# Performance work log

Hardware: AMD Instinct MI355X
Metric: run time of the kernel (lower is better)

## Reference

```python
import jax, jax.numpy as jnp
import numpy as np

N = 4096          # n_nodes == batch_size (GFN operates on dense [N,N] adjacency)
E = 65536         # edges per view (avg degree 16)
D = [512, 256, 128]
HV = [128, 64]    # hidden_size_v
HM = [64, 32]     # hidden_size


def _xavier(key, shape):
    fan_in, fan_out = shape[0], shape[1]
    lim = np.sqrt(6.0 / (fan_in + fan_out))
    return jax.random.uniform(key, shape, jnp.float32, -lim, lim)


def setup_inputs() -> dict:
    key = jax.random.key(0)
    ks = jax.random.split(key, 40)
    inp = {}
    inp['data1'] = jax.random.normal(ks[0], (N, D[0]), jnp.float32)
    inp['data2'] = jax.random.normal(ks[1], (N, D[1]), jnp.float32)
    inp['data3'] = jax.random.normal(ks[2], (N, D[2]), jnp.float32)
    # graphs: random edge lists + matching dense adjacency (g.ndata['adj'])
    for v, k_ in zip((1, 2, 3), (ks[3], ks[4], ks[5])):
        ka, kb = jax.random.split(k_)
        src = jax.random.randint(ka, (E,), 0, N, jnp.int32)
        dst = jax.random.randint(kb, (E,), 0, N, jnp.int32)
        adj = np.zeros((N, N), np.float32)
        adj[np.asarray(src), np.asarray(dst)] = 1.0
        inp[f'src{v}'] = src
        inp[f'dst{v}'] = dst
        inp[f'adj{v}'] = jnp.asarray(adj)
    # per-view GraphConv weights (DGL GraphConv: weight [in,out], bias [out])
    dims = {1: [D[0]] + HV, 2: [D[1]] + HV, 3: [D[2]] + HV}
    ki = 6
    for v in (1, 2, 3):
        for l in range(len(HV)):
            inp[f'w{v}_{l}'] = _xavier(ks[ki], (dims[v][l], dims[v][l + 1])); ki += 1
            inp[f'b{v}_{l}'] = jnp.zeros((dims[v][l + 1],), jnp.float32)
    # consensus GraphConv stack
    mdims = [HV[-1]] + HM
    for l in range(len(HM)):
        inp[f'wm_{l}'] = _xavier(ks[ki], (mdims[l], mdims[l + 1])); ki += 1
        inp[f'bm_{l}'] = jnp.zeros((mdims[l + 1],), jnp.float32)
    # FeatureFusion weights [HV[-1], HV[-1]]
    inp['fw1'] = _xavier(ks[ki], (HV[-1], HV[-1])); ki += 1
    inp['fw2'] = _xavier(ks[ki], (HV[-1], HV[-1])); ki += 1
    inp['fw3'] = _xavier(ks[ki], (HV[-1], HV[-1])); ki += 1
    # GFN: Linear(N, N//2) -> ReLU -> Linear(N//2, N); torch Linear weight [out,in]
    H = N // 2
    inp['gfn_w1'] = _xavier(ks[ki], (H, N)); ki += 1
    inp['gfn_b1'] = jnp.zeros((H,), jnp.float32)
    inp['gfn_w2'] = _xavier(ks[ki], (N, H)); ki += 1
    inp['gfn_b2'] = jnp.zeros((N,), jnp.float32)
    return inp


def _gconv(src, dst, x, W, b):
    ones = jnp.ones((src.shape[0],), x.dtype)
    deg_out = jnp.clip(jax.ops.segment_sum(ones, src, num_segments=N), 1.0)
    deg_in = jnp.clip(jax.ops.segment_sum(ones, dst, num_segments=N), 1.0)
    h = (x * jax.lax.rsqrt(deg_out)[:, None]) @ W  # diag norms commute with W
    agg = jax.ops.segment_sum(h[src], dst, num_segments=N)
    return agg * jax.lax.rsqrt(deg_in)[:, None] + b


def _dense_gconv(A, x, W, b):
    # same math on a dense (multigraph-count) adjacency; A[src,dst] counts edges
    deg_out = jnp.clip(A.sum(axis=1), 1.0)
    deg_in = jnp.clip(A.sum(axis=0), 1.0)
    h = (x * jax.lax.rsqrt(deg_out)[:, None]) @ W
    agg = A.T @ h
    return agg * jax.lax.rsqrt(deg_in)[:, None] + b


def reference(data1, data2, data3, src1, dst1, src2, dst2, src3, dst3,
              adj1, adj2, adj3,
              w1_0, b1_0, w1_1, b1_1, w2_0, b2_0, w2_1, b2_1,
              w3_0, b3_0, w3_1, b3_1, wm_0, bm_0, wm_1, bm_1,
              fw1, fw2, fw3, gfn_w1, gfn_b1, gfn_w2, gfn_b2):
    # per-view encoder stacks (relu on all but last layer)
    f1 = jax.nn.relu(_gconv(src1, dst1, data1, w1_0, b1_0))
    f1 = _gconv(src1, dst1, f1, w1_1, b1_1)
    f2 = jax.nn.relu(_gconv(src2, dst2, data2, w2_0, b2_0))
    f2 = _gconv(src2, dst2, f2, w2_1, b2_1)
    f3 = jax.nn.relu(_gconv(src3, dst3, data3, w3_0, b3_0))
    f3 = _gconv(src3, dst3, f3, w3_1, b3_1)
    # FeatureFusion (dropout treated as eval/identity): softmax then relu
    z = f1 @ fw1 + f2 @ fw2 + f3 @ fw3
    z = jax.nn.relu(jax.nn.softmax(z, axis=1))
    # consensus graph: GFN on summed dense adjacency
    adjin = adj1 + adj2 + adj3
    adj_r = jax.nn.relu(adjin @ gfn_w1.T + gfn_b1) @ gfn_w2.T + gfn_b2
    adj_p = jnp.round(jnp.clip(adj_r, 0.0, 1.0) + 0.1)
    # dgl.from_scipy on (adj_p + adj_p.T) keeps edge per nonzero; add_self_loop
    # adds one extra self edge per node -> multigraph edge counts = struct + I
    A = ((adj_p + adj_p.T) != 0).astype(jnp.float32) + jnp.eye(N, dtype=jnp.float32)
    A = jax.lax.stop_gradient(A)  # graph built from detached adj_p
    feat = jax.nn.relu(_dense_gconv(A, z, wm_0, bm_0))
    feat = _dense_gconv(A, feat, wm_1, bm_1)
    # InnerProductDecoder with identity activation (same for every view)
    adj_rec = feat @ feat.T
    return adj_r, adj_rec, feat
```

## Files before the change

kernel.cpp:

```cpp
#include <hip/hip_runtime.h>


#define N_ 4096
#define E_ 65536

typedef __attribute__((ext_vector_type(8))) short short8;
typedef __attribute__((ext_vector_type(4))) float f32x4;

__device__ __forceinline__ float bf2f(unsigned short u) {
  union { unsigned int i; float f; } v; v.i = ((unsigned int)u) << 16; return v.f;
}
__device__ __forceinline__ unsigned short f2bf(float f) {
  union { float f; unsigned int i; } v; v.f = f;
  return (unsigned short)((v.i + 0x7fffu + ((v.i >> 16) & 1u)) >> 16);
}

#define OFF_DEG    0
#define OFF_HX     28672
#define OFF_HBUF   552960
#define OFF_HBUF2  1077248
#define OFF_FV1    1339392
#define OFF_FV2    1601536
#define OFF_FV3    1863680
#define OFF_ZB     2125824
#define OFF_ZPRE   2387968
#define CSR_STRIDE 73732


__global__ void k_count3(const int* __restrict__ s1, const int* __restrict__ d1,
                         const int* __restrict__ s2, const int* __restrict__ d2,
                         const int* __restrict__ s3, const int* __restrict__ d3,
                         float* __restrict__ wd) {
  int v = blockIdx.x >> 8;
  int e = (blockIdx.x & 255) * 256 + threadIdx.x;
  const int* sv = v == 0 ? s1 : (v == 1 ? s2 : s3);
  const int* dv = v == 0 ? d1 : (v == 1 ? d2 : d3);
  atomicAdd(&wd[v * 8192 + sv[e]], 1.f);
  atomicAdd(&wd[v * 8192 + 4096 + dv[e]], 1.f);
}

__global__ void k_rsq(float* __restrict__ p, int n) {
  int i = blockIdx.x * 256 + threadIdx.x;
  if (i < n) p[i] = 1.f / sqrtf(fmaxf(p[i], 1.f));
}

__global__ void k_scan(const float* __restrict__ wd, int* __restrict__ csr) {
  int v = blockIdx.x;
  const float* di = wd + v * 8192 + 4096;
  int* ptr = csr + v * CSR_STRIDE;
  int* cur = ptr + 4100;
  __shared__ int part[256];
  int t = threadIdx.x;
  int local[16];
  int s = 0;
#pragma unroll
  for (int i = 0; i < 16; ++i) { local[i] = s; s += (int)di[t * 16 + i]; }
  part[t] = s;
  __syncthreads();
  for (int o = 1; o < 256; o <<= 1) {
    int x = (t >= o) ? part[t - o] : 0;
    __syncthreads();
    part[t] += x;
    __syncthreads();
  }
  int base = (t > 0) ? part[t - 1] : 0;
#pragma unroll
  for (int i = 0; i < 16; ++i) { ptr[t * 16 + i] = base + local[i]; cur[t * 16 + i] = 0; }
  if (t == 255) ptr[4096] = part[255];
}

__global__ void k_fill(const int* __restrict__ s1, const int* __restrict__ d1,
                       const int* __restrict__ s2, const int* __restrict__ d2,
                       const int* __restrict__ s3, const int* __restrict__ d3,
                       int* __restrict__ csr) {
  int v = blockIdx.x >> 8;
  int e = (blockIdx.x & 255) * 256 + threadIdx.x;
  const int* sv = v == 0 ? s1 : (v == 1 ? s2 : s3);
  const int* dv = v == 0 ? d1 : (v == 1 ? d2 : d3);
  int* ptr = csr + v * CSR_STRIDE;
  int* cur = ptr + 4100;
  int* cidx = cur + 4096;
  int d = dv[e];
  int pos = ptr[d] + atomicAdd(&cur[d], 1);
  cidx[pos] = sv[e];
}

template<int C, int RELU>
__global__ void k_agg(const float* __restrict__ h, const int* __restrict__ csrv,
                      const float* __restrict__ rs, const float* __restrict__ bias,
                      float* __restrict__ out) {
  const int* ptr = csrv;
  const int* cidx = csrv + 4100 + 4096;
  int wave = threadIdx.x >> 6, lane = threadIdx.x & 63;
  int dst, col;
  if (C == 128) { dst = (blockIdx.x << 1) + (wave >> 1); col = ((wave & 1) << 6) + lane; }
  else          { dst = (blockIdx.x << 2) + wave;        col = lane; }
  int e0 = ptr[dst], e1 = ptr[dst + 1];
  float acc = 0.f;
  for (int e = e0; e < e1; ++e) acc += h[(size_t)cidx[e] * C + col];
  float v = acc * rs[dst] + bias[col];
  if (RELU) v = fmaxf(v, 0.f);
  out[(size_t)dst * C + col] = v;
}

__global__ void k_bitset(const int* __restrict__ s1, const int* __restrict__ d1,
                         const int* __restrict__ s2, const int* __restrict__ d2,
                         const int* __restrict__ s3, const int* __restrict__ d3,
                         unsigned* __restrict__ bm) {
  int v = blockIdx.x >> 8;
  int e = (blockIdx.x & 255) * 256 + threadIdx.x;
  const int* sv = v == 0 ? s1 : (v == 1 ? s2 : s3);
  const int* dv = v == 0 ? d1 : (v == 1 ? d2 : d3);
  unsigned idx = (unsigned)sv[e] * 4096u + (unsigned)dv[e];
  atomicOr(&bm[v * 524288 + (idx >> 5)], 1u << (idx & 31));
}

__global__ void k_b2a(const unsigned* __restrict__ bm, ushort* __restrict__ adjin) {
  int i = blockIdx.x * 256 + threadIdx.x;
  int w = i >> 2, sh = (i & 3) << 3;
  unsigned a = bm[w] >> sh, b = bm[524288 + w] >> sh, c = bm[1048576 + w] >> sh;
  short8 o;
#pragma unroll
  for (int k = 0; k < 8; ++k) {
    int cnt = ((a >> k) & 1) + ((b >> k) & 1) + ((c >> k) & 1);
    o[k] = (short)f2bf((float)cnt);
  }
  *(short8*)(adjin + (size_t)i * 8) = o;
}

__global__ void k_split2(const float4* __restrict__ g1, const float4* __restrict__ g2,
                         ushort* __restrict__ w1h, ushort* __restrict__ w1l,
                         ushort* __restrict__ w2h, ushort* __restrict__ w2l) {
  int i = blockIdx.x * 256 + threadIdx.x;
  int hf = i >= 2097152;
  int j = hf ? i - 2097152 : i;
  float4 x = hf ? g2[j] : g1[j];
  ushort* ph = hf ? w2h : w1h;
  ushort* pl = hf ? w2l : w1l;
  ushort4 h, l;
  h.x = f2bf(x.x); l.x = f2bf(x.x - bf2f(h.x));
  h.y = f2bf(x.y); l.y = f2bf(x.y - bf2f(h.y));
  h.z = f2bf(x.z); l.z = f2bf(x.z - bf2f(h.z));
  h.w = f2bf(x.w); l.w = f2bf(x.w - bf2f(h.w));
  *(ushort4*)(ph + (size_t)j * 4) = h;
  *(ushort4*)(pl + (size_t)j * 4) = l;
}

template<int RELU, int WT>
__global__ void k_finalize(const float* __restrict__ agg, const float* __restrict__ rs,
                           const float* __restrict__ bias, float* __restrict__ out,
                           float* __restrict__ outT, int C) {
  int i = blockIdx.x * 256 + threadIdx.x;
  int row = i / C, c = i % C;
  if (row >= N_) return;
  float v = agg[i] * rs[row] + bias[c];
  if (RELU) v = fmaxf(v, 0.f);
  out[i] = v;
  if (WT) outT[(size_t)c * N_ + row] = v;
}

__global__ void k_softmax(const float* __restrict__ zp, float* __restrict__ z) {
  int row = blockIdx.x * 4 + (threadIdx.x >> 6);
  int lane = threadIdx.x & 63;
  float v = zp[row * 64 + lane];
  float m = v;
  for (int o = 32; o; o >>= 1) m = fmaxf(m, __shfl_xor(m, o, 64));
  float e = expf(v - m);
  float s = e;
  for (int o = 32; o; o >>= 1) s += __shfl_xor(s, o, 64);
  z[row * 64 + lane] = e / s;
}

__global__ void k_buildA(const float* __restrict__ adjr, ushort* __restrict__ Ab,
                         float* __restrict__ degA) {
  int bi = blockIdx.y, bj = blockIdx.x;
  __shared__ float t2[64][65];
  int t = threadIdx.x;
  for (int i = 0; i < 16; ++i) {
    int idx = t + i * 256, r = idx >> 6, c = idx & 63;
    t2[r][c] = adjr[(size_t)(bj * 64 + r) * N_ + bi * 64 + c];
  }
  __syncthreads();
  int w = t >> 6, lane = t & 63;
  for (int rr = 0; rr < 16; ++rr) {
    int r = w * 16 + rr;
    int gi = bi * 64 + r, gj = bj * 64 + lane;
    float p1 = rintf(fminf(fmaxf(adjr[(size_t)gi * N_ + gj], 0.f), 1.f) + 0.1f);
    float p2 = rintf(fminf(fmaxf(t2[lane][r], 0.f), 1.f) + 0.1f);
    float a = ((p1 + p2) != 0.f ? 1.f : 0.f) + (gi == gj ? 1.f : 0.f);
    Ab[(size_t)gi * N_ + gj] = f2bf(a);
    float s = a;
    for (int o = 32; o; o >>= 1) s += __shfl_xor(s, o, 64);
    if (lane == 0) atomicAdd(&degA[gi], s);
  }
}

template<int BN, int TM, int ABF16, int RS, int ATOM>
__global__ __launch_bounds__(256) void k_gemm(
    const void* __restrict__ Ap, int lda, const float* __restrict__ B, int ldb,
    float* __restrict__ C, int ldc, int K, const float* __restrict__ rs) {
  __shared__ float As[64][33];
  __shared__ float Bs[32][BN];
  const int t = threadIdx.x;
  const int bm = blockIdx.x << 6;
  const int bn = blockIdx.y * BN;
  const int Kc = K / gridDim.z;
  const int kbeg = blockIdx.z * Kc, kend = kbeg + Kc;
  const int cg = t % (BN / 4), rg = t / (BN / 4);
  float av[TM][4];
#pragma unroll
  for (int i = 0; i < TM; ++i)
#pragma unroll
    for (int j = 0; j < 4; ++j) av[i][j] = 0.f;
  for (int k0 = kbeg; k0 < kend; k0 += 32) {
    __syncthreads();
#pragma unroll
    for (int i = 0; i < 8; ++i) {
      int idx = t + (i << 8), r = idx >> 5, c = idx & 31;
      float v;
      if (ABF16) v = bf2f(((const ushort*)Ap)[(size_t)(bm + r) * lda + k0 + c]);
      else v = ((const float*)Ap)[(size_t)(bm + r) * lda + k0 + c];
      As[r][c] = v;
    }
#pragma unroll
    for (int i = 0; i < (BN >> 3); ++i) {
      int idx = t + (i << 8), r = idx / BN, c = idx % BN;
      Bs[r][c] = B[(size_t)(k0 + r) * ldb + bn + c];
    }
    __syncthreads();
#pragma unroll
    for (int k = 0; k < 32; ++k) {
      float b0 = Bs[k][(cg << 2) + 0], b1 = Bs[k][(cg << 2) + 1];
      float b2 = Bs[k][(cg << 2) + 2], b3 = Bs[k][(cg << 2) + 3];
#pragma unroll
      for (int i = 0; i < TM; ++i) {
        float a = As[rg * TM + i][k];
        av[i][0] = fmaf(a, b0, av[i][0]);
        av[i][1] = fmaf(a, b1, av[i][1]);
        av[i][2] = fmaf(a, b2, av[i][2]);
        av[i][3] = fmaf(a, b3, av[i][3]);
      }
    }
  }
#pragma unroll
  for (int i = 0; i < TM; ++i) {
    int gm = bm + rg * TM + i;
    float s = RS ? rs[gm] : 1.f;
#pragma unroll
    for (int j = 0; j < 4; ++j) {
      int gn = bn + (cg << 2) + j;
      float v = av[i][j] * s;
      if (ATOM) atomicAdd(&C[(size_t)gm * ldc + gn], v);
      else C[(size_t)gm * ldc + gn] = v;
    }
  }
}

template<int NA, int NB, int EPI>
__global__ __launch_bounds__(256, 2) void k_mfma(
    const ushort* __restrict__ A0, const ushort* __restrict__ A1,
    const ushort* __restrict__ B0, const ushort* __restrict__ B1,
    const float* __restrict__ bias, float* __restrict__ Cf,
    ushort* __restrict__ Oh, ushort* __restrict__ Ol, int Nn, int K) {
  constexpr int NOPS = NA + NB;
  __shared__ __align__(16) ushort lds[NOPS * 8192];
  const int t = threadIdx.x, lane = t & 63;
  const int wave = t >> 6, wm = wave >> 1, wn = wave & 1;
  const int bm = blockIdx.y << 7, bn = blockIdx.x << 7;
  const int hi = lane >> 4, r16 = lane & 15, rx = r16 & 7;
  const int srow = t >> 3, sslot = t & 7;

  const ushort* gsrc[4];
  int rb[4];
  {
    int no = 0;
    gsrc[no] = A0; rb[no] = bm; no++;
    if (NA > 1) { gsrc[no] = A1; rb[no] = bm; no++; }
    gsrc[no] = B0; rb[no] = bn; no++;
    if (NB > 1) { gsrc[no] = B1; rb[no] = bn; no++; }
  }

  f32x4 acc[4][4];
#pragma unroll
  for (int i = 0; i < 4; ++i)
#pragma unroll
    for (int j = 0; j < 4; ++j)
#pragma unroll
      for (int r = 0; r < 4; ++r) acc[i][j][r] = 0.f;

  short8 stg[NOPS][4];
#define LOADT(KT)                                                                      \
  {                                                                                    \
    _Pragma("unroll") for (int op = 0; op < NOPS; ++op)                                \
        _Pragma("unroll") for (int i = 0; i < 4; ++i) {                                \
      int row = (i << 5) + srow;                                                       \
      stg[op][i] = *(const short8*)(gsrc[op] + (size_t)(rb[op] + row) * K + (KT) +     \
                                    (sslot << 3));                                     \
    }                                                                                  \
  }

  LOADT(0);
  for (int kt = 0; kt < K; kt += 64) {
    __syncthreads();
#pragma unroll
    for (int op = 0; op < NOPS; ++op)
#pragma unroll
      for (int i = 0; i < 4; ++i) {
        int row = (i << 5) + srow;
        *(short8*)(&lds[op * 8192 + row * 64 + ((sslot ^ (row & 7)) << 3)]) = stg[op][i];
      }
    __syncthreads();
    if (kt + 64 < K) LOADT(kt + 64);
#pragma unroll
    for (int k0 = 0; k0 < 2; ++k0) {
      const int soff = (((k0 << 2) + hi) ^ rx) << 3;
      short8 af[NA][4], bf[NB][4];
#pragma unroll
      for (int mi = 0; mi < 4; ++mi) {
        int row = (wm << 6) + (mi << 4) + r16;
        af[0][mi] = *(const short8*)(&lds[row * 64 + soff]);
        if (NA > 1) af[1][mi] = *(const short8*)(&lds[8192 + row * 64 + soff]);
      }
#pragma unroll
      for (int ni = 0; ni < 4; ++ni) {
        int row = (wn << 6) + (ni << 4) + r16;
        bf[0][ni] = *(const short8*)(&lds[NA * 8192 + row * 64 + soff]);
        if (NB > 1) bf[1][ni] = *(const short8*)(&lds[(NA + 1) * 8192 + row * 64 + soff]);
      }
#pragma unroll
      for (int mi = 0; mi < 4; ++mi)
#pragma unroll
        for (int ni = 0; ni < 4; ++ni) {
          acc[mi][ni] = __builtin_amdgcn_mfma_f32_16x16x32_bf16(af[0][mi], bf[0][ni], acc[mi][ni], 0, 0, 0);
          if (NB > 1)
            acc[mi][ni] = __builtin_amdgcn_mfma_f32_16x16x32_bf16(af[0][mi], bf[1][ni], acc[mi][ni], 0, 0, 0);
          if (NA > 1)
            acc[mi][ni] = __builtin_amdgcn_mfma_f32_16x16x32_bf16(af[1][mi], bf[0][ni], acc[mi][ni], 0, 0, 0);
        }
    }
  }
#pragma unroll
  for (int mi = 0; mi < 4; ++mi)
#pragma unroll
    for (int ni = 0; ni < 4; ++ni) {
      const int gn = bn + (wn << 6) + (ni << 4) + r16;
      const float bv = bias[gn];
#pragma unroll
      for (int r2 = 0; r2 < 4; ++r2) {
        const int gm = bm + (wm << 6) + (mi << 4) + (hi << 2) + r2;
        float v = acc[mi][ni][r2] + bv;
        if (EPI == 1) {
          v = fmaxf(v, 0.f);
          ushort hh = f2bf(v);
          Oh[(size_t)gm * Nn + gn] = hh;
          Ol[(size_t)gm * Nn + gn] = f2bf(v - bf2f(hh));
        } else {
          Cf[(size_t)gm * Nn + gn] = v;
        }
      }
    }
}

extern "C" void kernel_launch(void* const* d_in, const int* in_sizes, int n_in,
                              void* d_out, int out_size, void* d_ws, size_t ws_size,
                              hipStream_t stream) {
  const float* data[3] = {(const float*)d_in[0], (const float*)d_in[1], (const float*)d_in[2]};
  const int D[3] = {512, 256, 128};
  const int* src[3] = {(const int*)d_in[3], (const int*)d_in[6], (const int*)d_in[9]};
  const int* dst[3] = {(const int*)d_in[4], (const int*)d_in[7], (const int*)d_in[10]};
  const float* w0[3] = {(const float*)d_in[12], (const float*)d_in[16], (const float*)d_in[20]};
  const float* b0[3] = {(const float*)d_in[13], (const float*)d_in[17], (const float*)d_in[21]};
  const float* w1[3] = {(const float*)d_in[14], (const float*)d_in[18], (const float*)d_in[22]};
  const float* b1[3] = {(const float*)d_in[15], (const float*)d_in[19], (const float*)d_in[23]};
  const float* wm0 = (const float*)d_in[24];
  const float* bm0 = (const float*)d_in[25];
  const float* wm1 = (const float*)d_in[26];
  const float* bm1 = (const float*)d_in[27];
  const float* fw[3] = {(const float*)d_in[28], (const float*)d_in[29], (const float*)d_in[30]};
  const float* gw1 = (const float*)d_in[31];
  const float* gb1 = (const float*)d_in[32];
  const float* gw2 = (const float*)d_in[33];
  const float* gb2 = (const float*)d_in[34];

  float* outf = (float*)d_out;
  float* adj_r = outf;
  float* adj_rec = outf + 16777216;
  float* feat = outf + 33554432;
  ushort* w1h = (ushort*)outf;
  ushort* w1l = w1h + 8388608;
  ushort* adjin = w1h + 16777216;
  ushort* o1u = (ushort*)adj_rec;
  ushort* h1h = o1u;
  ushort* h1l = o1u + 8388608;
  ushort* w2h = o1u + 16777216;
  ushort* w2l = o1u + 25165824;
  ushort* Ab = o1u;

  float* wsf = (float*)d_ws;
  float* degA = wsf + 24576;
  float* hX = wsf + OFF_HX;
  float* hbuf = wsf + OFF_HBUF;
  float* hbuf2 = wsf + OFF_HBUF2;
  float* fv[3] = {wsf + OFF_FV1, wsf + OFF_FV2, wsf + OFF_FV3};
  float* zb = wsf + OFF_ZB;
  float* zpre = wsf + OFF_ZPRE;
  int* csr = (int*)(wsf + OFF_ZPRE);
  unsigned* bm = (unsigned*)(wsf + OFF_HX);
  float* aggc = wsf + OFF_FV1;
  float* aggc2 = wsf + OFF_FV2;
  float* featT = wsf + OFF_FV3;

  hipMemsetAsync(wsf, 0, (size_t)1601536 * 4, stream);
  k_bitset<<<768, 256, 0, stream>>>(src[0], dst[0], src[1], dst[1], src[2], dst[2], bm);
  k_b2a<<<8192, 256, 0, stream>>>(bm, adjin);
  k_split2<<<16384, 256, 0, stream>>>((const float4*)gw1, (const float4*)gw2, w1h, w1l, w2h, w2l);
  k_mfma<1, 2, 1><<<dim3(16, 32), 256, 0, stream>>>(
      adjin, nullptr, w1h, w1l, gb1, nullptr, h1h, h1l, 2048, 4096);
  k_mfma<2, 2, 2><<<dim3(32, 32), 256, 0, stream>>>(
      h1h, h1l, w2h, w2l, gb2, adj_r, nullptr, nullptr, 4096, 2048);
  k_buildA<<<dim3(64, 64), 256, 0, stream>>>(adj_r, Ab, degA);

  k_count3<<<768, 256, 0, stream>>>(src[0], dst[0], src[1], dst[1], src[2], dst[2], wsf);
  k_scan<<<3, 256, 0, stream>>>(wsf, csr);
  k_rsq<<<112, 256, 0, stream>>>(wsf, 28672);
  k_fill<<<768, 256, 0, stream>>>(src[0], dst[0], src[1], dst[1], src[2], dst[2], csr);

  for (int v = 0; v < 3; ++v) {
    const float* rso = wsf + v * 8192;
    const float* rsi = wsf + v * 8192 + 4096;
    const int* csrv = csr + v * CSR_STRIDE;
    k_gemm<32, 2, 0, 1, 0><<<dim3(64, 4, 1), 256, 0, stream>>>(
        data[v], D[v], w0[v], 128, hX, 128, D[v], rso);
    k_agg<128, 1><<<2048, 256, 0, stream>>>(hX, csrv, rsi, b0[v], hbuf);
    k_gemm<32, 2, 0, 1, 0><<<dim3(64, 2, 1), 256, 0, stream>>>(
        hbuf, 128, w1[v], 64, hbuf2, 64, 128, rso);
    k_agg<64, 0><<<1024, 256, 0, stream>>>(hbuf2, csrv, rsi, b1[v], fv[v]);
  }
  k_gemm<32, 2, 0, 0, 0><<<dim3(64, 2, 1), 256, 0, stream>>>(
      fv[0], 64, fw[0], 64, zpre, 64, 64, nullptr);
  k_gemm<32, 2, 0, 0, 1><<<dim3(64, 2, 1), 256, 0, stream>>>(
      fv[1], 64, fw[1], 64, zpre, 64, 64, nullptr);
  k_gemm<32, 2, 0, 0, 1><<<dim3(64, 2, 1), 256, 0, stream>>>(
      fv[2], 64, fw[2], 64, zpre, 64, 64, nullptr);
  k_softmax<<<1024, 256, 0, stream>>>(zpre, zb);

  k_gemm<32, 2, 0, 1, 0><<<dim3(64, 2, 1), 256, 0, stream>>>(
      zb, 64, wm0, 64, hbuf2, 64, 64, degA);
  hipMemsetAsync(aggc, 0, (size_t)393216 * 4, stream);
  k_gemm<64, 4, 1, 0, 1><<<dim3(64, 1, 8), 256, 0, stream>>>(
      Ab, 4096, hbuf2, 64, aggc, 64, 4096, nullptr);
  k_finalize<1, 0><<<1024, 256, 0, stream>>>(aggc, degA, bm0, hbuf, nullptr, 64);
  k_gemm<32, 2, 0, 1, 0><<<dim3(64, 1, 1), 256, 0, stream>>>(
      hbuf, 64, wm1, 32, hbuf2, 32, 64, degA);
  k_gemm<32, 2, 1, 0, 1><<<dim3(64, 1, 8), 256, 0, stream>>>(
      Ab, 4096, hbuf2, 32, aggc2, 32, 4096, nullptr);
  k_finalize<0, 1><<<512, 256, 0, stream>>>(aggc2, degA, bm1, feat, featT, 32);
  k_gemm<128, 8, 0, 0, 0><<<dim3(64, 32, 1), 256, 0, stream>>>(
      feat, 32, featT, 4096, adj_rec, 4096, 32, nullptr);
}
```

Before: 1.048 ms.

## Move consensus dense aggregation to split-bf16 MFMA and fuse small prep kernels

The dense A·H aggregations in the consensus GraphConv stack now run on a new MFMA kernel. It uses hi/lo bf16 splits of the transposed features and a K-split into partial buffers that are reduced in a finalize kernel, replacing the scalar fp32 GEMM that used atomics. buildA now processes only upper-triangle tile pairs and writes the mirrored tile plus column degrees. Edge counting is merged with the bitset, bitset-to-adjacency is merged with the weight split, the scan is merged with rsqrt, and the three fusion GEMMs become one K=192 kernel. The change cuts launches, atomics and redundant adjacency reads, but adds transpose/split passes and rearranges workspace aliasing.

```diff
diff --git a/kernel.cpp b/kernel.cpp
--- a/kernel.cpp
+++ b/kernel.cpp
@@ -3,6 +3,7 @@
 
 #define N_ 4096
 #define E_ 65536
+#define CSR_STRIDE 73732
 
 typedef __attribute__((ext_vector_type(8))) short short8;
 typedef __attribute__((ext_vector_type(4))) float f32x4;
@@ -15,58 +16,89 @@
   return (unsigned short)((v.i + 0x7fffu + ((v.i >> 16) & 1u)) >> 16);
 }
 
-#define OFF_DEG    0
-#define OFF_HX     28672
-#define OFF_HBUF   552960
-#define OFF_HBUF2  1077248
-#define OFF_FV1    1339392
-#define OFF_FV2    1601536
-#define OFF_FV3    1863680
-#define OFF_ZB     2125824
-#define OFF_ZPRE   2387968
-#define CSR_STRIDE 73732
-
-
-__global__ void k_count3(const int* __restrict__ s1, const int* __restrict__ d1,
-                         const int* __restrict__ s2, const int* __restrict__ d2,
-                         const int* __restrict__ s3, const int* __restrict__ d3,
-                         float* __restrict__ wd) {
+__global__ void k_edges(const int* __restrict__ s1, const int* __restrict__ d1,
+                        const int* __restrict__ s2, const int* __restrict__ d2,
+                        const int* __restrict__ s3, const int* __restrict__ d3,
+                        float* __restrict__ wd, unsigned* __restrict__ bmp) {
   int v = blockIdx.x >> 8;
   int e = (blockIdx.x & 255) * 256 + threadIdx.x;
   const int* sv = v == 0 ? s1 : (v == 1 ? s2 : s3);
   const int* dv = v == 0 ? d1 : (v == 1 ? d2 : d3);
-  atomicAdd(&wd[v * 8192 + sv[e]], 1.f);
-  atomicAdd(&wd[v * 8192 + 4096 + dv[e]], 1.f);
-}
-
-__global__ void k_rsq(float* __restrict__ p, int n) {
+  int s = sv[e], d = dv[e];
+  atomicAdd(&wd[v * 8192 + s], 1.f);
+  atomicAdd(&wd[v * 8192 + 4096 + d], 1.f);
+  unsigned idx = (unsigned)s * 4096u + (unsigned)d;
+  atomicOr(&bmp[v * 524288 + (idx >> 5)], 1u << (idx & 31));
+}
+
+__global__ void k_prep(const unsigned* __restrict__ bmp, ushort* __restrict__ adjin,
+                       const float4* __restrict__ g1, const float4* __restrict__ g2,
+                       ushort* __restrict__ w1h, ushort* __restrict__ w1l,
+                       ushort* __restrict__ w2h, ushort* __restrict__ w2l) {
   int i = blockIdx.x * 256 + threadIdx.x;
-  if (i < n) p[i] = 1.f / sqrtf(fmaxf(p[i], 1.f));
-}
-
-__global__ void k_scan(const float* __restrict__ wd, int* __restrict__ csr) {
-  int v = blockIdx.x;
-  const float* di = wd + v * 8192 + 4096;
-  int* ptr = csr + v * CSR_STRIDE;
-  int* cur = ptr + 4100;
-  __shared__ int part[256];
-  int t = threadIdx.x;
-  int local[16];
-  int s = 0;
-#pragma unroll
-  for (int i = 0; i < 16; ++i) { local[i] = s; s += (int)di[t * 16 + i]; }
-  part[t] = s;
-  __syncthreads();
-  for (int o = 1; o < 256; o <<= 1) {
-    int x = (t >= o) ? part[t - o] : 0;
-    __syncthreads();
-    part[t] += x;
-    __syncthreads();
-  }
-  int base = (t > 0) ? part[t - 1] : 0;
-#pragma unroll
-  for (int i = 0; i < 16; ++i) { ptr[t * 16 + i] = base + local[i]; cur[t * 16 + i] = 0; }
-  if (t == 255) ptr[4096] = part[255];
+  if (i < 2097152) {
+    int w = i >> 2, sh = (i & 3) << 3;
+    unsigned a = bmp[w] >> sh, b = bmp[524288 + w] >> sh, c = bmp[1048576 + w] >> sh;
+    short8 o;
+#pragma unroll
+    for (int k = 0; k < 8; ++k) {
+      int cnt = ((a >> k) & 1) + ((b >> k) & 1) + ((c >> k) & 1);
+      o[k] = (short)f2bf((float)cnt);
+    }
+    *(short8*)(adjin + (size_t)i * 8) = o;
+  } else {
+    int i2 = i - 2097152;
+    int hf = i2 >= 2097152;
+    int j = i2 & 2097151;
+    float4 x = hf ? g2[j] : g1[j];
+    ushort* ph = hf ? w2h : w1h;
+    ushort* pl = hf ? w2l : w1l;
+    ushort4 h, l;
+    h.x = f2bf(x.x); l.x = f2bf(x.x - bf2f(h.x));
+    h.y = f2bf(x.y); l.y = f2bf(x.y - bf2f(h.y));
+    h.z = f2bf(x.z); l.z = f2bf(x.z - bf2f(h.z));
+    h.w = f2bf(x.w); l.w = f2bf(x.w - bf2f(h.w));
+    *(ushort4*)(ph + (size_t)j * 4) = h;
+    *(ushort4*)(pl + (size_t)j * 4) = l;
+  }
+}
+
+__global__ void k_scan7(float* __restrict__ wd, int* __restrict__ csr) {
+  int b = blockIdx.x, t = threadIdx.x;
+  if (b < 3) {
+    float* di = wd + b * 8192 + 4096;
+    int* ptr = csr + b * CSR_STRIDE;
+    int* cur = ptr + 4100;
+    __shared__ int part[256];
+    int local[16];
+    float cnt[16];
+    int s = 0;
+#pragma unroll
+    for (int i = 0; i < 16; ++i) { cnt[i] = di[t * 16 + i]; local[i] = s; s += (int)cnt[i]; }
+    part[t] = s;
+    __syncthreads();
+    for (int o = 1; o < 256; o <<= 1) {
+      int x = (t >= o) ? part[t - o] : 0;
+      __syncthreads();
+      part[t] += x;
+      __syncthreads();
+    }
+    int base = (t > 0) ? part[t - 1] : 0;
+#pragma unroll
+    for (int i = 0; i < 16; ++i) {
+      ptr[t * 16 + i] = base + local[i];
+      cur[t * 16 + i] = 0;
+      di[t * 16 + i] = 1.f / sqrtf(fmaxf(cnt[i], 1.f));
+    }
+    if (t == 255) ptr[4096] = part[255];
+  } else {
+    int off = (b == 3) ? 0 : (b == 4) ? 8192 : (b == 5) ? 16384 : 24576;
+#pragma unroll
+    for (int i = 0; i < 16; ++i) {
+      int idx = off + t * 16 + i;
+      wd[idx] = 1.f / sqrtf(fmaxf(wd[idx], 1.f));
+    }
+  }
 }
 
 __global__ void k_fill(const int* __restrict__ s1, const int* __restrict__ d1,
@@ -88,7 +120,7 @@
 template<int C, int RELU>
 __global__ void k_agg(const float* __restrict__ h, const int* __restrict__ csrv,
                       const float* __restrict__ rs, const float* __restrict__ bias,
-                      float* __restrict__ out) {
+                      float* __restrict__ out, int os, int oo) {
   const int* ptr = csrv;
   const int* cidx = csrv + 4100 + 4096;
   int wave = threadIdx.x >> 6, lane = threadIdx.x & 63;
@@ -100,63 +132,7 @@
   for (int e = e0; e < e1; ++e) acc += h[(size_t)cidx[e] * C + col];
   float v = acc * rs[dst] + bias[col];
   if (RELU) v = fmaxf(v, 0.f);
-  out[(size_t)dst * C + col] = v;
-}
-
-__global__ void k_bitset(const int* __restrict__ s1, const int* __restrict__ d1,
-                         const int* __restrict__ s2, const int* __restrict__ d2,
-                         const int* __restrict__ s3, const int* __restrict__ d3,
-                         unsigned* __restrict__ bm) {
-  int v = blockIdx.x >> 8;
-  int e = (blockIdx.x & 255) * 256 + threadIdx.x;
-  const int* sv = v == 0 ? s1 : (v == 1 ? s2 : s3);
-  const int* dv = v == 0 ? d1 : (v == 1 ? d2 : d3);
-  unsigned idx = (unsigned)sv[e] * 4096u + (unsigned)dv[e];
-  atomicOr(&bm[v * 524288 + (idx >> 5)], 1u << (idx & 31));
-}
-
-__global__ void k_b2a(const unsigned* __restrict__ bm, ushort* __restrict__ adjin) {
-  int i = blockIdx.x * 256 + threadIdx.x;
-  int w = i >> 2, sh = (i & 3) << 3;
-  unsigned a = bm[w] >> sh, b = bm[524288 + w] >> sh, c = bm[1048576 + w] >> sh;
-  short8 o;
-#pragma unroll
-  for (int k = 0; k < 8; ++k) {
-    int cnt = ((a >> k) & 1) + ((b >> k) & 1) + ((c >> k) & 1);
-    o[k] = (short)f2bf((float)cnt);
-  }
-  *(short8*)(adjin + (size_t)i * 8) = o;
-}
-
-__global__ void k_split2(const float4* __restrict__ g1, const float4* __restrict__ g2,
-                         ushort* __restrict__ w1h, ushort* __restrict__ w1l,
-                         ushort* __restrict__ w2h, ushort* __restrict__ w2l) {
-  int i = blockIdx.x * 256 + threadIdx.x;
-  int hf = i >= 2097152;
-  int j = hf ? i - 2097152 : i;
-  float4 x = hf ? g2[j] : g1[j];
-  ushort* ph = hf ? w2h : w1h;
-  ushort* pl = hf ? w2l : w1l;
-  ushort4 h, l;
-  h.x = f2bf(x.x); l.x = f2bf(x.x - bf2f(h.x));
-  h.y = f2bf(x.y); l.y = f2bf(x.y - bf2f(h.y));
-  h.z = f2bf(x.z); l.z = f2bf(x.z - bf2f(h.z));
-  h.w = f2bf(x.w); l.w = f2bf(x.w - bf2f(h.w));
-  *(ushort4*)(ph + (size_t)j * 4) = h;
-  *(ushort4*)(pl + (size_t)j * 4) = l;
-}
-
-template<int RELU, int WT>
-__global__ void k_finalize(const float* __restrict__ agg, const float* __restrict__ rs,
-                           const float* __restrict__ bias, float* __restrict__ out,
-                           float* __restrict__ outT, int C) {
-  int i = blockIdx.x * 256 + threadIdx.x;
-  int row = i / C, c = i % C;
-  if (row >= N_) return;
-  float v = agg[i] * rs[row] + bias[c];
-  if (RELU) v = fmaxf(v, 0.f);
-  out[i] = v;
-  if (WT) outT[(size_t)c * N_ + row] = v;
+  out[(size_t)dst * os + oo + col] = v;
 }
 
 __global__ void k_softmax(const float* __restrict__ zp, float* __restrict__ z) {
@@ -174,53 +150,66 @@
 __global__ void k_buildA(const float* __restrict__ adjr, ushort* __restrict__ Ab,
                          float* __restrict__ degA) {
   int bi = blockIdx.y, bj = blockIdx.x;
+  if (bi > bj) return;
   __shared__ float t2[64][65];
-  int t = threadIdx.x;
+  __shared__ ushort at[64][65];
+  __shared__ float cs[64];
+  int t = threadIdx.x, w = t >> 6, lane = t & 63;
+#pragma unroll
   for (int i = 0; i < 16; ++i) {
     int idx = t + i * 256, r = idx >> 6, c = idx & 63;
     t2[r][c] = adjr[(size_t)(bj * 64 + r) * N_ + bi * 64 + c];
   }
+  if (t < 64) cs[t] = 0.f;
   __syncthreads();
-  int w = t >> 6, lane = t & 63;
+  float colp = 0.f;
   for (int rr = 0; rr < 16; ++rr) {
     int r = w * 16 + rr;
     int gi = bi * 64 + r, gj = bj * 64 + lane;
     float p1 = rintf(fminf(fmaxf(adjr[(size_t)gi * N_ + gj], 0.f), 1.f) + 0.1f);
     float p2 = rintf(fminf(fmaxf(t2[lane][r], 0.f), 1.f) + 0.1f);
     float a = ((p1 + p2) != 0.f ? 1.f : 0.f) + (gi == gj ? 1.f : 0.f);
-    Ab[(size_t)gi * N_ + gj] = f2bf(a);
+    ushort ab = f2bf(a);
+    Ab[(size_t)gi * N_ + gj] = ab;
+    at[lane][r] = ab;
+    colp += a;
     float s = a;
     for (int o = 32; o; o >>= 1) s += __shfl_xor(s, o, 64);
     if (lane == 0) atomicAdd(&degA[gi], s);
   }
-}
-
-template<int BN, int TM, int ABF16, int RS, int ATOM>
+  if (bi < bj) {
+    atomicAdd(&cs[lane], colp);
+    __syncthreads();
+#pragma unroll
+    for (int i = 0; i < 16; ++i) {
+      int idx = t + i * 256, r = idx >> 6, c = idx & 63;
+      Ab[(size_t)(bj * 64 + r) * N_ + bi * 64 + c] = at[r][c];
+    }
+    if (t < 64) atomicAdd(&degA[bj * 64 + t], cs[t]);
+  }
+}
+
+template<int BN, int TM, int RS>
 __global__ __launch_bounds__(256) void k_gemm(
-    const void* __restrict__ Ap, int lda, const float* __restrict__ B, int ldb,
+    const float* __restrict__ Ap, int lda, const float* __restrict__ B, int ldb,
     float* __restrict__ C, int ldc, int K, const float* __restrict__ rs) {
   __shared__ float As[64][33];
   __shared__ float Bs[32][BN];
   const int t = threadIdx.x;
   const int bm = blockIdx.x << 6;
   const int bn = blockIdx.y * BN;
-  const int Kc = K / gridDim.z;
-  const int kbeg = blockIdx.z * Kc, kend = kbeg + Kc;
   const int cg = t % (BN / 4), rg = t / (BN / 4);
   float av[TM][4];
 #pragma unroll
   for (int i = 0; i < TM; ++i)
 #pragma unroll
     for (int j = 0; j < 4; ++j) av[i][j] = 0.f;
-  for (int k0 = kbeg; k0 < kend; k0 += 32) {
+  for (int k0 = 0; k0 < K; k0 += 32) {
     __syncthreads();
 #pragma unroll
     for (int i = 0; i < 8; ++i) {
       int idx = t + (i << 8), r = idx >> 5, c = idx & 31;
-      float v;
-      if (ABF16) v = bf2f(((const ushort*)Ap)[(size_t)(bm + r) * lda + k0 + c]);
-      else v = ((const float*)Ap)[(size_t)(bm + r) * lda + k0 + c];
-      As[r][c] = v;
+      As[r][c] = Ap[(size_t)(bm + r) * lda + k0 + c];
     }
 #pragma unroll
     for (int i = 0; i < (BN >> 3); ++i) {
@@ -247,13 +236,186 @@
     int gm = bm + rg * TM + i;
     float s = RS ? rs[gm] : 1.f;
 #pragma unroll
-    for (int j = 0; j < 4; ++j) {
-      int gn = bn + (cg << 2) + j;
-      float v = av[i][j] * s;
-      if (ATOM) atomicAdd(&C[(size_t)gm * ldc + gn], v);
-      else C[(size_t)gm * ldc + gn] = v;
-    }
-  }
+    for (int j = 0; j < 4; ++j)
+      C[(size_t)gm * ldc + bn + (cg << 2) + j] = av[i][j] * s;
+  }
+}
+
+__global__ __launch_bounds__(256) void k_fuse(
+    const float* __restrict__ Ap, const float* __restrict__ F1,
+    const float* __restrict__ F2, const float* __restrict__ F3,
+    float* __restrict__ C) {
+  __shared__ float As[64][33];
+  __shared__ float Bs[32][32];
+  const int t = threadIdx.x;
+  const int bm = blockIdx.x << 6;
+  const int bn = blockIdx.y * 32;
+  const int cg = t % 8, rg = t / 8;
+  float av[2][4];
+#pragma unroll
+  for (int i = 0; i < 2; ++i)
+#pragma unroll
+    for (int j = 0; j < 4; ++j) av[i][j] = 0.f;
+  for (int k0 = 0; k0 < 192; k0 += 32) {
+    __syncthreads();
+#pragma unroll
+    for (int i = 0; i < 8; ++i) {
+      int idx = t + (i << 8), r = idx >> 5, c = idx & 31;
+      As[r][c] = Ap[(size_t)(bm + r) * 192 + k0 + c];
+    }
+#pragma unroll
+    for (int i = 0; i < 4; ++i) {
+      int idx = t + (i << 8), r = idx >> 5, c = idx & 31;
+      int gr = k0 + r;
+      const float* Bp = gr < 64 ? F1 : (gr < 128 ? F2 : F3);
+      Bs[r][c] = Bp[(gr & 63) * 64 + bn + c];
+    }
+    __syncthreads();
+#pragma unroll
+    for (int k = 0; k < 32; ++k) {
+      float b0 = Bs[k][(cg << 2) + 0], b1 = Bs[k][(cg << 2) + 1];
+      float b2 = Bs[k][(cg << 2) + 2], b3 = Bs[k][(cg << 2) + 3];
+#pragma unroll
+      for (int i = 0; i < 2; ++i) {
+        float a = As[rg * 2 + i][k];
+        av[i][0] = fmaf(a, b0, av[i][0]);
+        av[i][1] = fmaf(a, b1, av[i][1]);
+        av[i][2] = fmaf(a, b2, av[i][2]);
+        av[i][3] = fmaf(a, b3, av[i][3]);
+      }
+    }
+  }
+#pragma unroll
+  for (int i = 0; i < 2; ++i)
+#pragma unroll
+    for (int j = 0; j < 4; ++j)
+      C[(size_t)(bm + rg * 2 + i) * 64 + bn + (cg << 2) + j] = av[i][j];
+}
+
+template<int C>
+__global__ void k_tsplit(const float* __restrict__ in, ushort* __restrict__ hTh,
+                         ushort* __restrict__ hTl) {
+  __shared__ float tl[64][C + 1];
+  int t = threadIdx.x;
+  int m0 = blockIdx.x * 64;
+#pragma unroll
+  for (int i = 0; i < (C >> 2); ++i) {
+    int idx = t + (i << 8), r = idx / C, c = idx % C;
+    tl[r][c] = in[(size_t)(m0 + r) * C + c];
+  }
+  __syncthreads();
+#pragma unroll
+  for (int i = 0; i < (C >> 2); ++i) {
+    int idx = t + (i << 8), c = idx >> 6, mm = idx & 63;
+    float v = tl[mm][c];
+    ushort hh = f2bf(v);
+    hTh[(size_t)c * N_ + m0 + mm] = hh;
+    hTl[(size_t)c * N_ + m0 + mm] = f2bf(v - bf2f(hh));
+  }
+}
+
+template<int BN>
+__global__ __launch_bounds__(256) void k_aggm(
+    const ushort* __restrict__ Ab, const ushort* __restrict__ hTh,
+    const ushort* __restrict__ hTl, float* __restrict__ part) {
+  constexpr int NF = BN / 16;
+  constexpr int BR = BN / 32;
+  __shared__ __align__(16) ushort lA[8192];
+  __shared__ __align__(16) ushort lBh[BN * 64];
+  __shared__ __align__(16) ushort lBl[BN * 64];
+  const int t = threadIdx.x, lane = t & 63, wave = t >> 6;
+  const int bm = blockIdx.x << 7;
+  const int kb = blockIdx.y << 9;
+  const int hi = lane >> 4, r16 = lane & 15, rx = r16 & 7;
+  const int srow = t >> 3, sslot = t & 7;
+
+  f32x4 acc[2][NF];
+#pragma unroll
+  for (int i = 0; i < 2; ++i)
+#pragma unroll
+    for (int j = 0; j < NF; ++j)
+#pragma unroll
+      for (int r = 0; r < 4; ++r) acc[i][j][r] = 0.f;
+
+  short8 sA[4], sBh[BR], sBl[BR];
+#define ALOAD(KT)                                                                     \
+  {                                                                                   \
+    _Pragma("unroll") for (int i = 0; i < 4; ++i) {                                   \
+      int row = (i << 5) + srow;                                                      \
+      sA[i] = *(const short8*)(Ab + (size_t)(bm + row) * 4096 + kb + (KT) + (sslot << 3)); \
+    }                                                                                 \
+    _Pragma("unroll") for (int i = 0; i < BR; ++i) {                                  \
+      int row = (i << 5) + srow;                                                      \
+      sBh[i] = *(const short8*)(hTh + (size_t)row * 4096 + kb + (KT) + (sslot << 3)); \
+      sBl[i] = *(const short8*)(hTl + (size_t)row * 4096 + kb + (KT) + (sslot << 3)); \
+    }                                                                                 \
+  }
+  ALOAD(0);
+  for (int kt = 0; kt < 512; kt += 64) {
+    __syncthreads();
+#pragma unroll
+    for (int i = 0; i < 4; ++i) {
+      int row = (i << 5) + srow;
+      *(short8*)(&lA[row * 64 + ((sslot ^ (row & 7)) << 3)]) = sA[i];
+    }
+#pragma unroll
+    for (int i = 0; i < BR; ++i) {
+      int row = (i << 5) + srow;
+      *(short8*)(&lBh[row * 64 + ((sslot ^ (row & 7)) << 3)]) = sBh[i];
+      *(short8*)(&lBl[row * 64 + ((sslot ^ (row & 7)) << 3)]) = sBl[i];
+    }
+    __syncthreads();
+    if (kt + 64 < 512) ALOAD(kt + 64);
+#pragma unroll
+    for (int k0 = 0; k0 < 2; ++k0) {
+      const int soff = (((k0 << 2) + hi) ^ rx) << 3;
+      short8 af[2], bh[NF], bl[NF];
+#pragma unroll
+      for (int mi = 0; mi < 2; ++mi) {
+        int row = wave * 32 + mi * 16 + r16;
+        af[mi] = *(const short8*)(&lA[row * 64 + soff]);
+      }
+#pragma unroll
+      for (int ni = 0; ni < NF; ++ni) {
+        int row = ni * 16 + r16;
+        bh[ni] = *(const short8*)(&lBh[row * 64 + soff]);
+        bl[ni] = *(const short8*)(&lBl[row * 64 + soff]);
+      }
+#pragma unroll
+      for (int mi = 0; mi < 2; ++mi)
+#pragma unroll
+        for (int ni = 0; ni < NF; ++ni) {
+          acc[mi][ni] = __builtin_amdgcn_mfma_f32_16x16x32_bf16(af[mi], bh[ni], acc[mi][ni], 0, 0, 0);
+          acc[mi][ni] = __builtin_amdgcn_mfma_f32_16x16x32_bf16(af[mi], bl[ni], acc[mi][ni], 0, 0, 0);
+        }
+    }
+  }
+#pragma unroll
+  for (int mi = 0; mi < 2; ++mi)
+#pragma unroll
+    for (int ni = 0; ni < NF; ++ni)
+#pragma unroll
+      for (int r2 = 0; r2 < 4; ++r2) {
+        int gm = bm + wave * 32 + mi * 16 + (hi << 2) + r2;
+        int gn = ni * 16 + r16;
+        part[((size_t)blockIdx.y * 4096 + gm) * BN + gn] = acc[mi][ni][r2];
+      }
+#undef ALOAD
+}
+
+template<int C, int RELU, int WFT>
+__global__ void k_fincons(const float* __restrict__ part, const float* __restrict__ rs,
+                          const float* __restrict__ bias, float* __restrict__ out,
+                          float* __restrict__ featT) {
+  int i = blockIdx.x * 256 + threadIdx.x;
+  int m = i / C, c = i % C;
+  float s = 0.f;
+#pragma unroll
+  for (int z = 0; z < 8; ++z) s += part[((size_t)z * 4096 + m) * C + c];
+  float v = s * rs[m] + bias[c];
+  if (RELU) v = fmaxf(v, 0.f);
+  out[i] = v;
+  if (WFT) featT[(size_t)c * N_ + m] = v;
 }
 
 template<int NA, int NB, int EPI>
@@ -359,6 +521,7 @@
         }
       }
     }
+#undef LOADT
 }
 
 extern "C" void kernel_launch(void* const* d_in, const int* in_sizes, int n_in,
@@ -398,63 +561,59 @@
 
   float* wsf = (float*)d_ws;
   float* degA = wsf + 24576;
-  float* hX = wsf + OFF_HX;
-  float* hbuf = wsf + OFF_HBUF;
-  float* hbuf2 = wsf + OFF_HBUF2;
-  float* fv[3] = {wsf + OFF_FV1, wsf + OFF_FV2, wsf + OFF_FV3};
-  float* zb = wsf + OFF_ZB;
-  float* zpre = wsf + OFF_ZPRE;
-  int* csr = (int*)(wsf + OFF_ZPRE);
-  unsigned* bm = (unsigned*)(wsf + OFF_HX);
-  float* aggc = wsf + OFF_FV1;
-  float* aggc2 = wsf + OFF_FV2;
-  float* featT = wsf + OFF_FV3;
+  unsigned* bmp = (unsigned*)(wsf + 28672);
+  float* hX = wsf + 28672;
+  float* hbuf = wsf + 552960;
+  float* t2 = wsf + 1077248;
+  float* fvI = wsf + 1339392;
+  int* csr = (int*)(wsf + 2125824);
+  float* zpre = wsf + 28672;
+  float* zb = wsf + 290816;
+  float* part0 = wsf + 552960;
+  float* t0 = wsf + 28672;
+  ushort* hT0h = (ushort*)(wsf + 290816);
+  ushort* hT0l = hT0h + 262144;
+  float* h1c = wsf + 28672;
+  float* t1 = wsf + 290816;
+  ushort* hT1h = (ushort*)(wsf + 421888);
+  ushort* hT1l = hT1h + 131072;
+  float* part1 = wsf + 552960;
+  float* featT = wsf + 28672;
 
   hipMemsetAsync(wsf, 0, (size_t)1601536 * 4, stream);
-  k_bitset<<<768, 256, 0, stream>>>(src[0], dst[0], src[1], dst[1], src[2], dst[2], bm);
-  k_b2a<<<8192, 256, 0, stream>>>(bm, adjin);
-  k_split2<<<16384, 256, 0, stream>>>((const float4*)gw1, (const float4*)gw2, w1h, w1l, w2h, w2l);
+  k_edges<<<768, 256, 0, stream>>>(src[0], dst[0], src[1], dst[1], src[2], dst[2], wsf, bmp);
+  k_prep<<<24576, 256, 0, stream>>>(bmp, adjin, (const float4*)gw1, (const float4*)gw2,
+                                    w1h, w1l, w2h, w2l);
   k_mfma<1, 2, 1><<<dim3(16, 32), 256, 0, stream>>>(
       adjin, nullptr, w1h, w1l, gb1, nullptr, h1h, h1l, 2048, 4096);
   k_mfma<2, 2, 2><<<dim3(32, 32), 256, 0, stream>>>(
       h1h, h1l, w2h, w2l, gb2, adj_r, nullptr, nullptr, 4096, 2048);
   k_buildA<<<dim3(64, 64), 256, 0, stream>>>(adj_r, Ab, degA);
 
-  k_count3<<<768, 256, 0, stream>>>(src[0], dst[0], src[1], dst[1], src[2], dst[2], wsf);
-  k_scan<<<3, 256, 0, stream>>>(wsf, csr);
-  k_rsq<<<112, 256, 0, stream>>>(wsf, 28672);
+  k_scan7<<<7, 256, 0, stream>>>(wsf, csr);
   k_fill<<<768, 256, 0, stream>>>(src[0], dst[0], src[1], dst[1], src[2], dst[2], csr);
-
   for (int v = 0; v < 3; ++v) {
     const float* rso = wsf + v * 8192;
     const float* rsi = wsf + v * 8192 + 4096;
     const int* csrv = csr + v * CSR_STRIDE;
-    k_gemm<32, 2, 0, 1, 0><<<dim3(64, 4, 1), 256, 0, stream>>>(
+    k_gemm<32, 2, 1><<<dim3(64, 4), 256, 0, stream>>>(
         data[v], D[v], w0[v], 128, hX, 128, D[v], rso);
-    k_agg<128, 1><<<2048, 256, 0, stream>>>(hX, csrv, rsi, b0[v], hbuf);
-    k_gemm<32, 2, 0, 1, 0><<<dim3(64, 2, 1), 256, 0, stream>>>(
-        hbuf, 128, w1[v], 64, hbuf2, 64, 128, rso);
-    k_agg<64, 0><<<1024, 256, 0, stream>>>(hbuf2, csrv, rsi, b1[v], fv[v]);
-  }
-  k_gemm<32, 2, 0, 0, 0><<<dim3(64, 2, 1), 256, 0, stream>>>(
-      fv[0], 64, fw[0], 64, zpre, 64, 64, nullptr);
-  k_gemm<32, 2, 0, 0, 1><<<dim3(64, 2, 1), 256, 0, stream>>>(
-      fv[1], 64, fw[1], 64, zpre, 64, 64, nullptr);
-  k_gemm<32, 2, 0, 0, 1><<<dim3(64, 2, 1), 256, 0, stream>>>(
-      fv[2], 64, fw[2], 64, zpre, 64, 64, nullptr);
+    k_agg<128, 1><<<2048, 256, 0, stream>>>(hX, csrv, rsi, b0[v], hbuf, 128, 0);
+    k_gemm<32, 2, 1><<<dim3(64, 2), 256, 0, stream>>>(
+        hbuf, 128, w1[v], 64, t2, 64, 128, rso);
+    k_agg<64, 0><<<1024, 256, 0, stream>>>(t2, csrv, rsi, b1[v], fvI, 192, v * 64);
+  }
+  k_fuse<<<dim3(64, 2), 256, 0, stream>>>(fvI, fw[0], fw[1], fw[2], zpre);
   k_softmax<<<1024, 256, 0, stream>>>(zpre, zb);
 
-  k_gemm<32, 2, 0, 1, 0><<<dim3(64, 2, 1), 256, 0, stream>>>(
-      zb, 64, wm0, 64, hbuf2, 64, 64, degA);
-  hipMemsetAsync(aggc, 0, (size_t)393216 * 4, stream);
-  k_gemm<64, 4, 1, 0, 1><<<dim3(64, 1, 8), 256, 0, stream>>>(
-      Ab, 4096, hbuf2, 64, aggc, 64, 4096, nullptr);
-  k_finalize<1, 0><<<1024, 256, 0, stream>>>(aggc, degA, bm0, hbuf, nullptr, 64);
-  k_gemm<32, 2, 0, 1, 0><<<dim3(64, 1, 1), 256, 0, stream>>>(
-      hbuf, 64, wm1, 32, hbuf2, 32, 64, degA);
-  k_gemm<32, 2, 1, 0, 1><<<dim3(64, 1, 8), 256, 0, stream>>>(
-      Ab, 4096, hbuf2, 32, aggc2, 32, 4096, nullptr);
-  k_finalize<0, 1><<<512, 256, 0, stream>>>(aggc2, degA, bm1, feat, featT, 32);
-  k_gemm<128, 8, 0, 0, 0><<<dim3(64, 32, 1), 256, 0, stream>>>(
+  k_gemm<32, 2, 1><<<dim3(64, 2), 256, 0, stream>>>(zb, 64, wm0, 64, t0, 64, 64, degA);
+  k_tsplit<64><<<64, 256, 0, stream>>>(t0, hT0h, hT0l);
+  k_aggm<64><<<dim3(32, 8), 256, 0, stream>>>(Ab, hT0h, hT0l, part0);
+  k_fincons<64, 1, 0><<<1024, 256, 0, stream>>>(part0, degA, bm0, h1c, nullptr);
+  k_gemm<32, 2, 1><<<dim3(64, 1), 256, 0, stream>>>(h1c, 64, wm1, 32, t1, 32, 64, degA);
+  k_tsplit<32><<<64, 256, 0, stream>>>(t1, hT1h, hT1l);
+  k_aggm<32><<<dim3(32, 8), 256, 0, stream>>>(Ab, hT1h, hT1l, part1);
+  k_fincons<32, 0, 1><<<512, 256, 0, stream>>>(part1, degA, bm1, feat, featT);
+  k_gemm<128, 8, 0><<<dim3(64, 32), 256, 0, stream>>>(
       feat, 32, featT, 4096, adj_rec, 4096, 32, nullptr);
 }
```

After: 952.1 us. 9.1% less time.
